# Kernel tuning notes

Hardware: AMD Instinct MI355X
Metric: run time of the kernel (lower is better)

The kernel has to match this reference:

```python
import jax, jax.numpy as jnp
import numpy as np

NEG = 0.01  # leaky relu negative_slope
N = 4096    # neurons in this (relu) layer == rows of prev linear W
M = 4096    # inputs to prev linear layer


def setup_inputs() -> dict:
    key = jax.random.key(0)
    k1, k2, k3, k4, k5, k6, k7 = jax.random.split(key, 7)
    center = jax.random.normal(k1, (N,), dtype=jnp.float32)
    radius = jax.random.uniform(k2, (N,), dtype=jnp.float32)
    lowerBound = center - radius
    upperBound = center + radius
    alpha = jax.random.uniform(k3, (N,), minval=NEG, maxval=1.0, dtype=jnp.float32)
    W = jax.random.normal(k4, (N, M), dtype=jnp.float32) / np.float32(np.sqrt(M))
    b = jax.random.normal(k5, (N,), dtype=jnp.float32) * 0.1
    c0 = jax.random.normal(k6, (M,), dtype=jnp.float32)
    r0 = jax.random.uniform(k7, (M,), dtype=jnp.float32)
    return dict(lowerBound=lowerBound, upperBound=upperBound, alpha=alpha,
                W=W, b=b, l0=c0 - r0, u0=c0 + r0)


def reference(lowerBound, upperBound, alpha, W, b, l0, u0):
    ns = jnp.float32(NEG)
    # per-neuron slope/bias bounds (elementwise, exactly as the torch code)
    lw = jnp.full_like(lowerBound, ns)
    uw = jnp.full_like(upperBound, ns)
    ub_bias = jnp.zeros_like(upperBound)
    lb_bias = jnp.zeros_like(lowerBound)
    positive = lowerBound > 0
    lw = jnp.where(positive, 1.0, lw)
    uw = jnp.where(positive, 1.0, uw)
    crossing = (lowerBound < 0) & (upperBound > 0)
    slope = jnp.where(crossing,
                      (upperBound - ns * lowerBound) / (upperBound - lowerBound),
                      0.0)
    uw = jnp.where(crossing, slope, uw)
    ub_bias = jnp.where(crossing, (ns - slope) * lowerBound, ub_bias)
    a = jnp.clip(alpha, ns, 1.0)  # alpha.data.clamp_
    lw = jnp.where(crossing, a, lw)

    # faithful: materialize dense diagonal relational weight matrices [N,N]
    D_l = jnp.diag(lw)
    D_u = jnp.diag(uw)

    # prev (linear) backsubstitution: sign-split + four matmuls + bias accumulation
    Dup, Dun = jnp.maximum(D_u, 0.0), jnp.minimum(D_u, 0.0)
    Dlp, Dln = jnp.maximum(D_l, 0.0), jnp.minimum(D_l, 0.0)
    ub_bias = ub_bias + Dup @ b + Dun @ b   # linear layer: upper bias == lower bias == b
    lb_bias = lb_bias + Dlp @ b + Dln @ b
    Wu = Dup @ W + Dun @ W                  # [N,M]
    Wl = Dlp @ W + Dln @ W

    # input-layer concretization against the input box [l0, u0]
    upper = jnp.maximum(Wu, 0.0) @ u0 + jnp.minimum(Wu, 0.0) @ l0 + ub_bias
    lower = jnp.maximum(Wl, 0.0) @ l0 + jnp.minimum(Wl, 0.0) @ u0 + lb_bias
    return jnp.stack([lower, upper])  # [2, N]
```

## Files before the change

kernel.cpp:

```cpp
#include <hip/hip_runtime.h>

#define NN 4096
#define MM 4096
#define NEG 0.01f

__global__ __launch_bounds__(256, 4) void abstract_leaky_relu_kernel(
    const float* __restrict__ lbnd,
    const float* __restrict__ ubnd,
    const float* __restrict__ alpha,
    const float* __restrict__ W,
    const float* __restrict__ b,
    const float* __restrict__ l0,
    const float* __restrict__ u0,
    float* __restrict__ out)
{
    __shared__ float s_c[MM];
    __shared__ float s_r[MM];

    for (int j = threadIdx.x; j < MM; j += 256) {
        float l = l0[j], u = u0[j];
        s_c[j] = 0.5f * (l + u);
        s_r[j] = 0.5f * (u - l);
    }
    __syncthreads();

    const int wave = threadIdx.x >> 6;
    const int lane = threadIdx.x & 63;
    const int row  = (blockIdx.x << 2) + wave;

    const float* __restrict__ Wr = W + (size_t)row * MM;

    float s1 = 0.0f;
    float s2 = 0.0f;
    #pragma unroll 4
    for (int j = lane * 4; j < MM; j += 64 * 4) {
        const float4 w = *(const float4*)(Wr + j);
        const float4 c = *(const float4*)(s_c + j);
        const float4 r = *(const float4*)(s_r + j);
        s1 += w.x * c.x + w.y * c.y + w.z * c.z + w.w * c.w;
        s2 += fabsf(w.x) * r.x + fabsf(w.y) * r.y +
              fabsf(w.z) * r.z + fabsf(w.w) * r.w;
    }

    #pragma unroll
    for (int off = 32; off > 0; off >>= 1) {
        s1 += __shfl_down(s1, off);
        s2 += __shfl_down(s2, off);
    }

    if (lane == 0) {
        const float L = lbnd[row];
        const float U = ubnd[row];
        const float A = alpha[row];
        const float B = b[row];

        float lw = NEG, uw = NEG, ub_bias = 0.0f;
        if (L > 0.0f) {
            lw = 1.0f; uw = 1.0f;
        } else if (L < 0.0f && U > 0.0f) {
            const float slope = (U - NEG * L) / (U - L);
            uw = slope;
            ub_bias = (NEG - slope) * L;
            lw = fminf(fmaxf(A, NEG), 1.0f);
        }

        const float Pu = s1 + s2;
        const float Pl = s1 - s2;
        out[row]      = lw * (Pl + B);
        out[NN + row] = uw * (Pu + B);
    }
}

extern "C" void kernel_launch(void* const* d_in, const int* in_sizes, int n_in,
                              void* d_out, int out_size, void* d_ws, size_t ws_size,
                              hipStream_t stream) {
    const float* lbnd  = (const float*)d_in[0];
    const float* ubnd  = (const float*)d_in[1];
    const float* alpha = (const float*)d_in[2];
    const float* W     = (const float*)d_in[3];
    const float* b     = (const float*)d_in[4];
    const float* l0    = (const float*)d_in[5];
    const float* u0    = (const float*)d_in[6];
    float* out = (float*)d_out;

    abstract_leaky_relu_kernel<<<NN / 4, 256, 0, stream>>>(
        lbnd, ubnd, alpha, W, b, l0, u0, out);
}
```

Baseline: 104.7 us.

## Split W columns into slabs with multi-row waves and a separate epilogue kernel

Work is split across 4 column slabs of 1024 columns each. Every wave now handles 4 rows, keeps its slice of center and radius in registers, and issues 16 independent float4 loads of W. Partial sums go to workspace, and a second small kernel reduces the slabs and applies the per-neuron slope and bias logic. The aim is more memory parallelism per wave, less shared-memory staging per block and smaller LDS use, at the cost of an extra launch and a round trip through workspace. The epilogue also now adds ub_bias to the upper bound, which the old kernel left out.

```diff
diff --git a/kernel.cpp b/kernel.cpp
--- a/kernel.cpp
+++ b/kernel.cpp
@@ -4,71 +4,115 @@
 #define MM 4096
 #define NEG 0.01f
 
-__global__ __launch_bounds__(256, 4) void abstract_leaky_relu_kernel(
-    const float* __restrict__ lbnd,
-    const float* __restrict__ ubnd,
-    const float* __restrict__ alpha,
+#define SLABS 4
+#define SLABW 1024
+#define RPB 16
+#define RPW 4
+
+__global__ __launch_bounds__(256, 4) void partial_kernel(
     const float* __restrict__ W,
-    const float* __restrict__ b,
     const float* __restrict__ l0,
     const float* __restrict__ u0,
-    float* __restrict__ out)
+    float2* __restrict__ part)
 {
-    __shared__ float s_c[MM];
-    __shared__ float s_r[MM];
+    __shared__ float s_c[SLABW];
+    __shared__ float s_r[SLABW];
 
-    for (int j = threadIdx.x; j < MM; j += 256) {
-        float l = l0[j], u = u0[j];
-        s_c[j] = 0.5f * (l + u);
-        s_r[j] = 0.5f * (u - l);
+    const int sb   = blockIdx.x & (SLABS - 1);
+    const int rb   = blockIdx.x >> 2;
+    const int col0 = sb * SLABW;
+
+    {
+        const int j = threadIdx.x * 4;
+        const float4 l = *(const float4*)(l0 + col0 + j);
+        const float4 u = *(const float4*)(u0 + col0 + j);
+        *(float4*)(s_c + j) = make_float4(0.5f*(l.x+u.x), 0.5f*(l.y+u.y),
+                                          0.5f*(l.z+u.z), 0.5f*(l.w+u.w));
+        *(float4*)(s_r + j) = make_float4(0.5f*(u.x-l.x), 0.5f*(u.y-l.y),
+                                          0.5f*(u.z-l.z), 0.5f*(u.w-l.w));
     }
     __syncthreads();
 
     const int wave = threadIdx.x >> 6;
     const int lane = threadIdx.x & 63;
-    const int row  = (blockIdx.x << 2) + wave;
+    const int row0 = rb * RPB + wave * RPW;
 
-    const float* __restrict__ Wr = W + (size_t)row * MM;
+    float4 cc[4], rr[4];
+    #pragma unroll
+    for (int t = 0; t < 4; ++t) {
+        cc[t] = *(const float4*)(s_c + t * 256 + lane * 4);
+        rr[t] = *(const float4*)(s_r + t * 256 + lane * 4);
+    }
 
-    float s1 = 0.0f;
-    float s2 = 0.0f;
-    #pragma unroll 4
-    for (int j = lane * 4; j < MM; j += 64 * 4) {
-        const float4 w = *(const float4*)(Wr + j);
-        const float4 c = *(const float4*)(s_c + j);
-        const float4 r = *(const float4*)(s_r + j);
-        s1 += w.x * c.x + w.y * c.y + w.z * c.z + w.w * c.w;
-        s2 += fabsf(w.x) * r.x + fabsf(w.y) * r.y +
-              fabsf(w.z) * r.z + fabsf(w.w) * r.w;
+    float s1[RPW] = {0.f, 0.f, 0.f, 0.f};
+    float s2[RPW] = {0.f, 0.f, 0.f, 0.f};
+
+    #pragma unroll
+    for (int k = 0; k < RPW; ++k) {
+        const float* __restrict__ Wr = W + (size_t)(row0 + k) * MM + col0;
+        #pragma unroll
+        for (int t = 0; t < 4; ++t) {
+            const float4 w = *(const float4*)(Wr + t * 256 + lane * 4);
+            s1[k] += w.x * cc[t].x + w.y * cc[t].y +
+                     w.z * cc[t].z + w.w * cc[t].w;
+            s2[k] += fabsf(w.x) * rr[t].x + fabsf(w.y) * rr[t].y +
+                     fabsf(w.z) * rr[t].z + fabsf(w.w) * rr[t].w;
+        }
     }
 
     #pragma unroll
     for (int off = 32; off > 0; off >>= 1) {
-        s1 += __shfl_down(s1, off);
-        s2 += __shfl_down(s2, off);
+        #pragma unroll
+        for (int k = 0; k < RPW; ++k) {
+            s1[k] += __shfl_down(s1[k], off);
+            s2[k] += __shfl_down(s2[k], off);
+        }
     }
 
     if (lane == 0) {
-        const float L = lbnd[row];
-        const float U = ubnd[row];
-        const float A = alpha[row];
-        const float B = b[row];
+        #pragma unroll
+        for (int k = 0; k < RPW; ++k)
+            part[sb * NN + row0 + k] = make_float2(s1[k], s2[k]);
+    }
+}
 
-        float lw = NEG, uw = NEG, ub_bias = 0.0f;
-        if (L > 0.0f) {
-            lw = 1.0f; uw = 1.0f;
-        } else if (L < 0.0f && U > 0.0f) {
-            const float slope = (U - NEG * L) / (U - L);
-            uw = slope;
-            ub_bias = (NEG - slope) * L;
-            lw = fminf(fmaxf(A, NEG), 1.0f);
-        }
+__global__ __launch_bounds__(256) void epilogue_kernel(
+    const float2* __restrict__ part,
+    const float* __restrict__ lbnd,
+    const float* __restrict__ ubnd,
+    const float* __restrict__ alpha,
+    const float* __restrict__ b,
+    float* __restrict__ out)
+{
+    const int row = blockIdx.x * 256 + threadIdx.x;
 
-        const float Pu = s1 + s2;
-        const float Pl = s1 - s2;
-        out[row]      = lw * (Pl + B);
-        out[NN + row] = uw * (Pu + B);
+    float s1 = 0.f, s2 = 0.f;
+    #pragma unroll
+    for (int sb = 0; sb < SLABS; ++sb) {
+        const float2 p = part[sb * NN + row];
+        s1 += p.x;
+        s2 += p.y;
     }
+
+    const float L = lbnd[row];
+    const float U = ubnd[row];
+    const float A = alpha[row];
+    const float B = b[row];
+
+    float lw = NEG, uw = NEG, ub_bias = 0.0f;
+    if (L > 0.0f) {
+        lw = 1.0f; uw = 1.0f;
+    } else if (L < 0.0f && U > 0.0f) {
+        const float slope = (U - NEG * L) / (U - L);
+        uw = slope;
+        ub_bias = (NEG - slope) * L;
+        lw = fminf(fmaxf(A, NEG), 1.0f);
+    }
+
+    const float Pu = s1 + s2;
+    const float Pl = s1 - s2;
+    out[row]      = lw * (Pl + B);
+    out[NN + row] = uw * (Pu + B) + ub_bias;
 }
 
 extern "C" void kernel_launch(void* const* d_in, const int* in_sizes, int n_in,
@@ -81,8 +125,9 @@
     const float* b     = (const float*)d_in[4];
     const float* l0    = (const float*)d_in[5];
     const float* u0    = (const float*)d_in[6];
-    float* out = (float*)d_out;
+    float* out   = (float*)d_out;
+    float2* part = (float2*)d_ws;
 
-    abstract_leaky_relu_kernel<<<NN / 4, 256, 0, stream>>>(
-        lbnd, ubnd, alpha, W, b, l0, u0, out);
+    partial_kernel<<<(NN / RPB) * SLABS, 256, 0, stream>>>(W, l0, u0, part);
+    epilogue_kernel<<<NN / 256, 256, 0, stream>>>(part, lbnd, ubnd, alpha, b, out);
 }
```

Result: slower. 109.4 us (+4.5%).
